# Performance work log

Hardware: AMD Instinct MI355X
Metric: run time of the kernel (lower is better)

The kernel has to match this reference:

```python
import jax, jax.numpy as jnp
import numpy as np

N_STATE = 4      # d_state from CrossMambaFusionBlock(d_state=4)
DT_RANK = 48     # ceil(768/16), standard Mamba dt_rank='auto'
D_CONV = 4       # depthwise causal conv kernel size


def _ln(x, g, b):
    m = jnp.mean(x, axis=-1, keepdims=True)
    v = jnp.mean((x - m) ** 2, axis=-1, keepdims=True)
    return (x - m) * jax.lax.rsqrt(v + 1e-5) * g + b


def _dwconv1d(u, w, b):
    # u: (B,L,D); w: (D,1,K) depthwise causal conv along token dim L
    K = w.shape[-1]
    up = jnp.pad(jnp.transpose(u, (0, 2, 1)), ((0, 0), (0, 0), (K - 1, 0)))
    out = jax.lax.conv_general_dilated(up, w, (1,), 'VALID',
                                       feature_group_count=w.shape[0],
                                       dimension_numbers=('NCH', 'OIH', 'NCH'))
    return jnp.transpose(out, (0, 2, 1)) + b


def _pre(x, g, b, Win, Wconv, bconv, Wxp, Wdt, bdt):
    # LayerNorm -> in_proj -> depthwise conv + SiLU -> dt/B/C projections
    B_, H, W, C = x.shape
    xn = _ln(x, g, b).reshape(B_, H * W, C)
    u, z = jnp.split(xn @ Win, 2, axis=-1)              # (B,L,D) each
    u = jax.nn.silu(_dwconv1d(u, Wconv, bconv))
    dbl = u @ Wxp                                        # (B,L,R+2N)
    dtr, Bm, Cm = jnp.split(dbl, [DT_RANK, DT_RANK + N_STATE], axis=-1)
    dt = jax.nn.softplus(dtr @ Wdt + bdt)                # (B,L,D)
    return u, z, dt, Bm, Cm


def _selective_scan(u, dt, Alog, Bm, Cm, Dskip):
    # u, dt: (B,L,D); Alog: (D,N); Bm, Cm: (B,L,N)
    A = -jnp.exp(Alog)
    dA = jnp.exp(dt[..., None] * A)                      # (B,L,D,N) decay
    dBu = (dt * u)[..., None] * Bm[:, :, None, :]        # (B,L,D,N) input

    def comb(c1, c2):
        a1, h1 = c1
        a2, h2 = c2
        return a1 * a2, a2 * h1 + h2

    _, h = jax.lax.associative_scan(comb, (dA, dBu), axis=1)
    return jnp.einsum('bldn,bln->bld', h, Cm) + u * Dskip


def _forward(x1, x2,
             ln_g1, ln_b1, Win1, Wconv1, bconv1, Wxp1, Wdt1, bdt1, Alog1, Dskip1, Wout1,
             ln_g2, ln_b2, Win2, Wconv2, bconv2, Wxp2, Wdt2, bdt2, Alog2, Dskip2, Wout2):
    x1 = jnp.transpose(x1, (0, 2, 3, 1))  # BCHW -> BHWC (as in forward_features)
    x2 = jnp.transpose(x2, (0, 2, 3, 1))
    B_, H, W, C = x1.shape
    u1, z1, dt1, B1, C1 = _pre(x1, ln_g1, ln_b1, Win1, Wconv1, bconv1, Wxp1, Wdt1, bdt1)
    u2, z2, dt2, B2, C2 = _pre(x2, ln_g2, ln_b2, Win2, Wconv2, bconv2, Wxp2, Wdt2, bdt2)
    # Cross-modal fusion: each stream's SSM state is read out with the OTHER
    # stream's C projection (cross selective scan).
    y1 = _selective_scan(u1, dt1, Alog1, B1, C2, Dskip1)
    y2 = _selective_scan(u2, dt2, Alog2, B2, C1, Dskip2)
    o1 = ((y1 * jax.nn.silu(z1)) @ Wout1).reshape(B_, H, W, C)
    o2 = ((y2 * jax.nn.silu(z2)) @ Wout2).reshape(B_, H, W, C)
    return x1 + o1, x2 + o2


def setup_inputs():
    key = jax.random.key(0)
    ks = jax.random.split(key, 16)
    B_, C, H, W = 2, 768, 64, 64
    D = C  # d_inner (ssm_ratio = 1)

    def nrm(k, shape, s=0.02):
        return jax.random.normal(k, shape, jnp.float32) * s

    inp = {
        'x1': jax.random.normal(ks[0], (B_, C, H, W), jnp.float32),
        'x2': jax.random.normal(ks[1], (B_, C, H, W), jnp.float32),
    }
    for i, o in ((1, 2), (2, 8)):
        inp[f'ln_g{i}'] = jnp.ones((C,), jnp.float32)
        inp[f'ln_b{i}'] = jnp.zeros((C,), jnp.float32)
        inp[f'Win{i}'] = nrm(ks[o], (C, 2 * D))
        inp[f'Wconv{i}'] = nrm(ks[o + 1], (D, 1, D_CONV), 0.1)
        inp[f'bconv{i}'] = jnp.zeros((D,), jnp.float32)
        inp[f'Wxp{i}'] = nrm(ks[o + 2], (D, DT_RANK + 2 * N_STATE))
        inp[f'Wdt{i}'] = nrm(ks[o + 3], (DT_RANK, D), 0.05)
        inp[f'bdt{i}'] = jnp.full((D,), -4.6, jnp.float32)  # softplus -> dt ~ 0.01
        inp[f'Alog{i}'] = jnp.log(jnp.broadcast_to(
            jnp.arange(1, N_STATE + 1, dtype=jnp.float32), (D, N_STATE)))
        inp[f'Dskip{i}'] = jnp.ones((D,), jnp.float32)
        inp[f'Wout{i}'] = nrm(ks[o + 4], (D, C))
    return inp


def reference(x1, x2,
              ln_g1, ln_b1, Win1, Wconv1, bconv1, Wxp1, Wdt1, bdt1, Alog1, Dskip1, Wout1,
              ln_g2, ln_b2, Win2, Wconv2, bconv2, Wxp2, Wdt2, bdt2, Alog2, Dskip2, Wout2):
    return _forward(x1, x2,
                    ln_g1, ln_b1, Win1, Wconv1, bconv1, Wxp1, Wdt1, bdt1, Alog1, Dskip1, Wout1,
                    ln_g2, ln_b2, Win2, Wconv2, bconv2, Wxp2, Wdt2, bdt2, Alog2, Dskip2, Wout2)
```

## Files before the change

### kernel.cpp

```cpp
#include <hip/hip_runtime.h>
#include <cmath>

#define LDIM 4096
#define CDIM 768
#define BDIM 2
#define NST 4
#define RNK 48
#define CH 64
#define LC 64
#define NDT 896

typedef short bf16x8 __attribute__((ext_vector_type(8)));
typedef float f32x4 __attribute__((ext_vector_type(4)));

__device__ __forceinline__ float sigmoidf_(float x) { return 1.f / (1.f + __expf(-x)); }

__device__ __forceinline__ unsigned short f2bf(float f) {
    unsigned int u = __float_as_uint(f);
    u += 0x7fffu + ((u >> 16) & 1u);
    return (unsigned short)(u >> 16);
}
__device__ __forceinline__ float bf2f(unsigned short us) {
    unsigned int u = ((unsigned int)us) << 16;
    return __uint_as_float(u);
}

__device__ __forceinline__ void llds16(const unsigned short* g, unsigned short* l) {
    __builtin_amdgcn_global_load_lds(
        (const __attribute__((address_space(1))) unsigned int*)g,
        (__attribute__((address_space(3))) unsigned int*)l, 16, 0, 0);
}

__global__ __launch_bounds__(256) void stats_kernel(const float* __restrict__ x0,
                                                    const float* __restrict__ x1,
                                                    float* __restrict__ stats)
{
    int blk = blockIdx.x;
    int s = blk >> 7;
    int b = (blk >> 6) & 1;
    int l0 = (blk & 63) * 64;
    int wave = threadIdx.x >> 6, lane = threadIdx.x & 63;
    const float* x = s ? x1 : x0;
    const float* xp = x + ((size_t)b * CDIM) * LDIM + l0 + lane;
    float sm = 0.f, sq = 0.f;
    int cbeg = wave * 192;
#pragma unroll
    for (int i0 = 0; i0 < 192; i0 += 16) {
        float v[16];
#pragma unroll
        for (int j = 0; j < 16; j++) v[j] = xp[(size_t)(cbeg + i0 + j) * LDIM];
#pragma unroll
        for (int j = 0; j < 16; j++) { sm += v[j]; sq += v[j] * v[j]; }
    }
    __shared__ float red[2][4][64];
    red[0][wave][lane] = sm;
    red[1][wave][lane] = sq;
    __syncthreads();
    if (wave == 0) {
        float s_ = red[0][0][lane] + red[0][1][lane] + red[0][2][lane] + red[0][3][lane];
        float q_ = red[1][0][lane] + red[1][1][lane] + red[1][2][lane] + red[1][3][lane];
        float m = s_ * (1.f / CDIM);
        float var = q_ * (1.f / CDIM) - m * m;
        int idx = s * 8192 + b * LDIM + l0 + lane;
        stats[2 * idx] = m;
        stats[2 * idx + 1] = rsqrtf(var + 1e-5f);
    }
}

__global__ __launch_bounds__(256) void transpose_ln_kernel(
    const float* __restrict__ x0, const float* __restrict__ x1,
    const float* __restrict__ g0, const float* __restrict__ bb0,
    const float* __restrict__ g1, const float* __restrict__ bb1,
    const float* __restrict__ stats,
    unsigned short* __restrict__ xnb0, unsigned short* __restrict__ xnb1,
    float* __restrict__ out)
{
    __shared__ float tile[64][65];
    int t = threadIdx.x;
    int c0 = blockIdx.x * 64, l0 = blockIdx.y * 64;
    int z = blockIdx.z;
    int s = z >> 1, b = z & 1;
    const float* x = s ? x1 : x0;
    const float* g = s ? g1 : g0;
    const float* bb = s ? bb1 : bb0;
    unsigned short* xnb = s ? xnb1 : xnb0;
    int tl = t & 63, tg = t >> 6;
#pragma unroll
    for (int i = 0; i < 16; i++) {
        int cl = tg * 16 + i;
        tile[cl][tl] = x[((size_t)(b * CDIM + c0 + cl)) * LDIM + l0 + tl];
    }
    __syncthreads();
    const size_t SZ = (size_t)BDIM * LDIM * CDIM;
#pragma unroll
    for (int i = 0; i < 16; i++) {
        int ll = tg * 16 + i;
        int l = l0 + ll, c = c0 + tl;
        float v = tile[tl][ll];
        int sidx = s * 8192 + b * LDIM + l;
        float m = stats[sidx * 2], rs = stats[sidx * 2 + 1];
        size_t o = ((size_t)(b * LDIM + l)) * CDIM + c;
        out[(size_t)s * SZ + o] = v;
        xnb[o] = f2bf((v - m) * rs * g[c] + bb[c]);
    }
}

__global__ __launch_bounds__(256) void wt_transpose_all(
    const float* __restrict__ Win0, const float* __restrict__ Win1,
    const float* __restrict__ Wout0, const float* __restrict__ Wout1,
    unsigned short* __restrict__ WinT0, unsigned short* __restrict__ WinT1,
    unsigned short* __restrict__ WoutT0, unsigned short* __restrict__ WoutT1)
{
    int z = blockIdx.z;
    const float* W = (z == 0) ? Win0 : (z == 1) ? Win1 : (z == 2) ? Wout0 : Wout1;
    unsigned short* Wt = (z == 0) ? WinT0 : (z == 1) ? WinT1 : (z == 2) ? WoutT0 : WoutT1;
    const int K = CDIM;
    const int N = (z < 2) ? 2 * CDIM : CDIM;
    if (blockIdx.x * 64 >= N) return;
    __shared__ float tile[64][65];
    int t = threadIdx.x;
    int n0 = blockIdx.x * 64, k0 = blockIdx.y * 64;
    int tn = t & 63, tg = t >> 6;
#pragma unroll
    for (int i = 0; i < 16; i++) {
        int kl = tg * 16 + i;
        tile[kl][tn] = W[(size_t)(k0 + kl) * N + n0 + tn];
    }
    __syncthreads();
#pragma unroll
    for (int i = 0; i < 16; i++) {
        int nl = tg * 16 + i;
        int k = k0 + tn, n = n0 + nl;
        Wt[(size_t)n * K + k] = f2bf(tile[tn][nl]);
    }
}

__global__ __launch_bounds__(256) void wcomb_kernel(
    const float* __restrict__ Wxp0, const float* __restrict__ Wdt0,
    const float* __restrict__ Wxp1, const float* __restrict__ Wdt1,
    unsigned short* __restrict__ W0, unsigned short* __restrict__ W1)
{
    int s = blockIdx.z;
    const float* Wxp = s ? Wxp1 : Wxp0;
    const float* Wdt = s ? Wdt1 : Wdt0;
    unsigned short* WcombT = s ? W1 : W0;
    int t = threadIdx.x;
    int k = blockIdx.x * 64 + (t & 63);
    int n0 = blockIdx.y * 64;
    float wx[RNK];
#pragma unroll
    for (int r = 0; r < RNK; r++) wx[r] = Wxp[k * 56 + r];
    for (int i = (t >> 6); i < 64; i += 4) {
        int n = n0 + i;
        float val;
        if (n < CDIM) {
            float acc = 0.f;
#pragma unroll
            for (int r = 0; r < RNK; r++) acc += wx[r] * Wdt[(size_t)r * CDIM + n];
            val = acc;
        } else if (n < CDIM + 8) {
            val = Wxp[k * 56 + RNK + (n - CDIM)];
        } else {
            val = 0.f;
        }
        WcombT[(size_t)n * CDIM + k] = f2bf(val);
    }
}

__global__ __launch_bounds__(512, 4) void gemm_mfma(
    const unsigned short* __restrict__ A0, const unsigned short* __restrict__ A1,
    const unsigned short* __restrict__ Bt0, const unsigned short* __restrict__ Bt1,
    void* __restrict__ C0, void* __restrict__ C1, int ldc, int K, int epi,
    const float* __restrict__ bias0, const float* __restrict__ bias1,
    float* __restrict__ D0, float* __restrict__ D1)
{
    const unsigned short* A = blockIdx.z ? A1 : A0;
    const unsigned short* Bt = blockIdx.z ? Bt1 : Bt0;
    void* C = blockIdx.z ? C1 : C0;
    const float* bias = blockIdx.z ? bias1 : bias0;
    float* D = blockIdx.z ? D1 : D0;

    __shared__ unsigned short As[3][128 * 32];
    __shared__ unsigned short Bs[3][128 * 32];
    const int tid = threadIdx.x;
    const int wave = tid >> 6, lane = tid & 63;
    const int row0 = blockIdx.x * 128, col0 = blockIdx.y * 128;
    const int wm = (wave >> 2) * 64, wn = (wave & 3) * 32;
    f32x4 acc[4][2] = {};
    const int lr = lane >> 2;
    const int gi = ((lane & 3) ^ ((lane >> 3) & 3)) * 8;
    const int fr = lane & 15, fc = lane >> 4;

    const unsigned short* ga0 = A + (size_t)(row0 + wave * 16 + lr) * K + gi;
    const unsigned short* gb0 = Bt + (size_t)(col0 + wave * 16 + lr) * K + gi;
    const int rb = wave * 16;

#define ISSUE(st, kb)                         \
    do {                                      \
        llds16(ga0 + (kb), &As[st][rb * 32]); \
        llds16(gb0 + (kb), &Bs[st][rb * 32]); \
    } while (0)

    const int NIT = K / 32;
    ISSUE(0, 0);
    ISSUE(1, 32);
    for (int i = 0; i < NIT; i++) {
        if (i < NIT - 1) __builtin_amdgcn_s_waitcnt(0xF72);
        else __builtin_amdgcn_s_waitcnt(0xF70);
        __builtin_amdgcn_s_barrier();
        if (i + 2 < NIT) ISSUE((i + 2) % 3, (i + 2) * 32);
        const unsigned short* as = As[i % 3];
        const unsigned short* bs = Bs[i % 3];
        bf16x8 af[4], bfr[2];
#pragma unroll
        for (int ii = 0; ii < 4; ii++) {
            int r = wm + ii * 16 + fr;
            af[ii] = *(const bf16x8*)&as[r * 32 + (fc ^ ((r >> 1) & 3)) * 8];
        }
#pragma unroll
        for (int j = 0; j < 2; j++) {
            int r = wn + j * 16 + fr;
            bfr[j] = *(const bf16x8*)&bs[r * 32 + (fc ^ ((r >> 1) & 3)) * 8];
        }
#pragma unroll
        for (int ii = 0; ii < 4; ii++)
#pragma unroll
            for (int j = 0; j < 2; j++)
                acc[ii][j] = __builtin_amdgcn_mfma_f32_16x16x32_bf16(af[ii], bfr[j], acc[ii][j], 0, 0, 0);
    }
#undef ISSUE

    const int cr = (lane >> 4) * 4, cc = lane & 15;
#pragma unroll
    for (int ii = 0; ii < 4; ii++)
#pragma unroll
        for (int j = 0; j < 2; j++) {
            int col = col0 + wn + j * 16 + cc;
#pragma unroll
            for (int r = 0; r < 4; r++) {
                int row = row0 + wm + ii * 16 + cr + r;
                float v = acc[ii][j][r];
                if (epi == 1) {
                    float* Cf = (float*)C;
                    size_t o = (size_t)row * ldc + col;
                    Cf[o] = v + Cf[o];
                } else if (epi == 2) {
                    if (col < CDIM) {
                        v += bias[col];
                        v = (v > 20.f) ? v : __logf(1.f + __expf(v));
                        ((unsigned short*)C)[(size_t)row * ldc + col] = f2bf(v);
                    } else if (col < CDIM + 8) {
                        D[(size_t)row * 8 + (col - CDIM)] = v;
                    }
                } else {
                    ((unsigned short*)C)[(size_t)row * ldc + col] = f2bf(v);
                }
            }
        }
}

__global__ __launch_bounds__(256) void conv_silu_kernel(
    const unsigned short* __restrict__ uzb0, const unsigned short* __restrict__ uzb1,
    const float* __restrict__ w0, const float* __restrict__ bc0,
    const float* __restrict__ w1, const float* __restrict__ bc1,
    unsigned short* __restrict__ ub0, unsigned short* __restrict__ ub1)
{
    int s = blockIdx.y;
    const unsigned short* uzb = s ? uzb1 : uzb0;
    const float* w = s ? w1 : w0;
    const float* bc = s ? bc1 : bc0;
    unsigned short* ub = s ? ub1 : ub0;
    int idx = blockIdx.x * 256 + threadIdx.x;
    int d8 = (idx % 96) * 8;
    int bl = idx / 96;
    int l = bl & (LDIM - 1);

    float wr[8][4];
#pragma unroll
    for (int q = 0; q < 8; q++) {
        f32x4 wv = *(const f32x4*)&w[(d8 + q) * 4];
#pragma unroll
        for (int k = 0; k < 4; k++) wr[q][k] = wv[k];
    }
    float acc[8];
    f32x4 b0 = *(const f32x4*)&bc[d8];
    f32x4 b1 = *(const f32x4*)&bc[d8 + 4];
#pragma unroll
    for (int q = 0; q < 4; q++) { acc[q] = b0[q]; acc[4 + q] = b1[q]; }

#pragma unroll
    for (int k = 0; k < 4; k++) {
        int ls = l - 3 + k;
        if (ls >= 0) {
            bf16x8 uv = *(const bf16x8*)&uzb[(size_t)(bl - 3 + k) * (2 * CDIM) + d8];
#pragma unroll
            for (int q = 0; q < 8; q++)
                acc[q] += bf2f((unsigned short)uv[q]) * wr[q][k];
        }
    }
    bf16x8 ov;
#pragma unroll
    for (int q = 0; q < 8; q++) {
        float v = acc[q];
        ov[q] = (short)f2bf(v * sigmoidf_(v));
    }
    *(bf16x8*)&ub[(size_t)bl * CDIM + d8] = ov;
}

__global__ __launch_bounds__(256) void scan_phaseA(
    const unsigned short* __restrict__ u0, const unsigned short* __restrict__ dt0,
    const float* __restrict__ dbl0, const float* __restrict__ Alog0,
    const unsigned short* __restrict__ u1, const unsigned short* __restrict__ dt1,
    const float* __restrict__ dbl1, const float* __restrict__ Alog1,
    float* __restrict__ agg)
{
    int idx = blockIdx.x * 256 + threadIdx.x;
    int d = idx % CDIM;
    int t1 = idx / CDIM;
    int c = t1 % CH;
    int t2 = t1 / CH;
    int b = t2 & 1;
    int s = t2 >> 1;
    const unsigned short* u = s ? u1 : u0;
    const unsigned short* dt = s ? dt1 : dt0;
    const float* dbl = s ? dbl1 : dbl0;
    const float* Alog = s ? Alog1 : Alog0;
    float A[4];
#pragma unroll
    for (int n = 0; n < 4; n++) A[n] = -__expf(Alog[d * 4 + n]);
    float h[4] = {0, 0, 0, 0}, aa[4] = {1, 1, 1, 1};
    int rowb = b * LDIM + c * LC;
    for (int t = 0; t < LC; t++) {
        int row = rowb + t;
        float dtv = bf2f(dt[(size_t)row * CDIM + d]);
        float uv = bf2f(u[(size_t)row * CDIM + d]);
        float du = dtv * uv;
        const float* bm = dbl + (size_t)row * 8;
#pragma unroll
        for (int n = 0; n < 4; n++) {
            float dA = __expf(dtv * A[n]);
            h[n] = dA * h[n] + du * bm[n];
            aa[n] *= dA;
        }
    }
    float* o = agg + (size_t)idx * 8;
#pragma unroll
    for (int n = 0; n < 4; n++) { o[n] = aa[n]; o[4 + n] = h[n]; }
}

__global__ __launch_bounds__(256) void scan_phaseB(const float* __restrict__ agg,
                                                   float* __restrict__ hinit)
{
    int idx = blockIdx.x * 256 + threadIdx.x;
    int d = idx % CDIM;
    int sb = idx / CDIM;
    float st[4] = {0, 0, 0, 0};
    for (int c = 0; c < CH; c++) {
        size_t base = ((size_t)sb * CH + c) * CDIM + d;
        const float* a = agg + base * 8;
        float* hi = hinit + base * 4;
#pragma unroll
        for (int n = 0; n < 4; n++) hi[n] = st[n];
#pragma unroll
        for (int n = 0; n < 4; n++) st[n] = a[n] * st[n] + a[4 + n];
    }
}

__global__ __launch_bounds__(256) void scan_phaseC(
    const unsigned short* __restrict__ u0, const unsigned short* __restrict__ dt0,
    const unsigned short* __restrict__ uzb0, const float* __restrict__ dbl0,
    const float* __restrict__ Alog0, const float* __restrict__ Dsk0, unsigned short* __restrict__ g0,
    const unsigned short* __restrict__ u1, const unsigned short* __restrict__ dt1,
    const unsigned short* __restrict__ uzb1, const float* __restrict__ dbl1,
    const float* __restrict__ Alog1, const float* __restrict__ Dsk1, unsigned short* __restrict__ g1,
    const float* __restrict__ hinit)
{
    int idx = blockIdx.x * 256 + threadIdx.x;
    int d = idx % CDIM;
    int t1 = idx / CDIM;
    int c = t1 % CH;
    int t2 = t1 / CH;
    int b = t2 & 1;
    int s = t2 >> 1;
    const unsigned short* u = s ? u1 : u0;
    const unsigned short* dt = s ? dt1 : dt0;
    const unsigned short* uzb = s ? uzb1 : uzb0;
    const float* dbl = s ? dbl1 : dbl0;
    const float* dblO = s ? dbl0 : dbl1;
    const float* Alog = s ? Alog1 : Alog0;
    const float* Dsk = s ? Dsk1 : Dsk0;
    unsigned short* gated = s ? g1 : g0;
    float A[4];
#pragma unroll
    for (int n = 0; n < 4; n++) A[n] = -__expf(Alog[d * 4 + n]);
    float Dv = Dsk[d];
    float h[4];
    const float* hi = hinit + (size_t)idx * 4;
#pragma unroll
    for (int n = 0; n < 4; n++) h[n] = hi[n];
    int rowb = b * LDIM + c * LC;
    for (int t = 0; t < LC; t++) {
        int row = rowb + t;
        float dtv = bf2f(dt[(size_t)row * CDIM + d]);
        float uv = bf2f(u[(size_t)row * CDIM + d]);
        float du = dtv * uv;
        const float* bm = dbl + (size_t)row * 8;
        const float* cm = dblO + (size_t)row * 8 + 4;
        float y = 0.f;
#pragma unroll
        for (int n = 0; n < 4; n++) {
            float dA = __expf(dtv * A[n]);
            h[n] = dA * h[n] + du * bm[n];
            y += h[n] * cm[n];
        }
        y += uv * Dv;
        float zv = bf2f(uzb[(size_t)row * (2 * CDIM) + CDIM + d]);
        gated[(size_t)row * CDIM + d] = f2bf(y * (zv * sigmoidf_(zv)));
    }
}

extern "C" void kernel_launch(void* const* d_in, const int* in_sizes, int n_in,
                              void* d_out, int out_size, void* d_ws, size_t ws_size,
                              hipStream_t stream)
{
    const float* x[2] = {(const float*)d_in[0], (const float*)d_in[1]};
    const float *ln_g[2], *ln_b[2], *Win[2], *Wconv[2], *bconv[2], *Wxp[2],
        *Wdt[2], *bdt[2], *Alog[2], *Dskip[2], *Wout[2];
    for (int s = 0; s < 2; s++) {
        int base = 2 + s * 11;
        ln_g[s] = (const float*)d_in[base + 0];
        ln_b[s] = (const float*)d_in[base + 1];
        Win[s] = (const float*)d_in[base + 2];
        Wconv[s] = (const float*)d_in[base + 3];
        bconv[s] = (const float*)d_in[base + 4];
        Wxp[s] = (const float*)d_in[base + 5];
        Wdt[s] = (const float*)d_in[base + 6];
        bdt[s] = (const float*)d_in[base + 7];
        Alog[s] = (const float*)d_in[base + 8];
        Dskip[s] = (const float*)d_in[base + 9];
        Wout[s] = (const float*)d_in[base + 10];
    }

    const int M = BDIM * LDIM;
    char* base = (char*)d_ws;
    auto alloc = [&](size_t bytes) {
        char* p = base;
        base += (bytes + 255) & ~(size_t)255;
        return p;
    };
    unsigned short* uzb[2] = {(unsigned short*)alloc((size_t)M * 1536 * 2),
                              (unsigned short*)alloc((size_t)M * 1536 * 2)};
    unsigned short* dtb[2] = {(unsigned short*)alloc((size_t)M * CDIM * 2),
                              (unsigned short*)alloc((size_t)M * CDIM * 2)};
    unsigned short* ub[2] = {(unsigned short*)alloc((size_t)M * CDIM * 2),
                             (unsigned short*)alloc((size_t)M * CDIM * 2)};
    unsigned short* xnb[2] = {(unsigned short*)alloc((size_t)M * CDIM * 2),
                              (unsigned short*)alloc((size_t)M * CDIM * 2)};
    float* dbl[2] = {(float*)alloc((size_t)M * 8 * 4), (float*)alloc((size_t)M * 8 * 4)};
    unsigned short* WinT[2] = {(unsigned short*)alloc(1536 * 768 * 2),
                               (unsigned short*)alloc(1536 * 768 * 2)};
    unsigned short* WoutT[2] = {(unsigned short*)alloc(768 * 768 * 2),
                                (unsigned short*)alloc(768 * 768 * 2)};
    unsigned short* WcombT[2] = {(unsigned short*)alloc((size_t)NDT * 768 * 2),
                                 (unsigned short*)alloc((size_t)NDT * 768 * 2)};
    float* agg = (float*)alloc((size_t)2 * BDIM * CH * CDIM * 8 * 4);
    float* hinit = (float*)alloc((size_t)2 * BDIM * CH * CDIM * 4 * 4);
    float* stats = (float*)alloc((size_t)2 * M * 2 * 4);

    dim3 blk(256);
    dim3 blk512(512);
    const size_t SZ = (size_t)BDIM * LDIM * CDIM;

    stats_kernel<<<dim3(256), blk, 0, stream>>>(x[0], x[1], stats);
    transpose_ln_kernel<<<dim3(CDIM / 64, LDIM / 64, 4), blk, 0, stream>>>(
        x[0], x[1], ln_g[0], ln_b[0], ln_g[1], ln_b[1], stats, xnb[0], xnb[1], (float*)d_out);

    wt_transpose_all<<<dim3(1536 / 64, 768 / 64, 4), blk, 0, stream>>>(
        Win[0], Win[1], Wout[0], Wout[1], WinT[0], WinT[1], WoutT[0], WoutT[1]);
    wcomb_kernel<<<dim3(768 / 64, NDT / 64, 2), blk, 0, stream>>>(
        Wxp[0], Wdt[0], Wxp[1], Wdt[1], WcombT[0], WcombT[1]);

    gemm_mfma<<<dim3(M / 128, 1536 / 128, 2), blk512, 0, stream>>>(
        xnb[0], xnb[1], WinT[0], WinT[1], uzb[0], uzb[1], 2 * CDIM, CDIM, 3,
        nullptr, nullptr, nullptr, nullptr);

    conv_silu_kernel<<<dim3((M * CDIM / 8) / 256, 2), blk, 0, stream>>>(
        uzb[0], uzb[1], Wconv[0], bconv[0], Wconv[1], bconv[1], ub[0], ub[1]);

    gemm_mfma<<<dim3(M / 128, NDT / 128, 2), blk512, 0, stream>>>(
        ub[0], ub[1], WcombT[0], WcombT[1], dtb[0], dtb[1], CDIM, CDIM, 2,
        bdt[0], bdt[1], dbl[0], dbl[1]);

    scan_phaseA<<<dim3((2 * BDIM * CH * CDIM) / 256), blk, 0, stream>>>(
        ub[0], dtb[0], dbl[0], Alog[0], ub[1], dtb[1], dbl[1], Alog[1], agg);
    scan_phaseB<<<dim3((2 * BDIM * CDIM) / 256), blk, 0, stream>>>(agg, hinit);
    scan_phaseC<<<dim3((2 * BDIM * CH * CDIM) / 256), blk, 0, stream>>>(
        ub[0], dtb[0], uzb[0], dbl[0], Alog[0], Dskip[0], xnb[0],
        ub[1], dtb[1], uzb[1], dbl[1], Alog[1], Dskip[1], xnb[1], hinit);

    float* out = (float*)d_out;
    gemm_mfma<<<dim3(M / 128, CDIM / 128, 2), blk512, 0, stream>>>(
        xnb[0], xnb[1], WoutT[0], WoutT[1], out, out + SZ, CDIM, CDIM, 1,
        nullptr, nullptr, nullptr, nullptr);
}
```

Baseline: 435.0 us.

## Merge prep kernels, vectorize transpose loads, and process two channels per scan thread

Folds the stats, weight-transpose and combined-weight kernels into one prep launch dispatched by block index, cutting two kernel launches. The LayerNorm transpose kernel now reads x with 16-byte vector loads instead of scalar loads. The scan phase A and C kernels each handle two adjacent channels per thread using 32-bit packed bf16 loads and stores, which halves the thread count and amortizes the per-row B/C loads. The scan changes lower parallelism, which may reduce latency hiding in the scans.

Measured after the change: 423.7 us. 1.03x faster.

```diff
diff --git a/kernel.cpp b/kernel.cpp
--- a/kernel.cpp
+++ b/kernel.cpp
@@ -24,6 +24,8 @@
     unsigned int u = ((unsigned int)us) << 16;
     return __uint_as_float(u);
 }
+__device__ __forceinline__ float bf2f_lo(unsigned int p) { return __uint_as_float(p << 16); }
+__device__ __forceinline__ float bf2f_hi(unsigned int p) { return __uint_as_float(p & 0xffff0000u); }
 
 __device__ __forceinline__ void llds16(const unsigned short* g, unsigned short* l) {
     __builtin_amdgcn_global_load_lds(
@@ -31,39 +33,103 @@
         (__attribute__((address_space(3))) unsigned int*)l, 16, 0, 0);
 }
 
-__global__ __launch_bounds__(256) void stats_kernel(const float* __restrict__ x0,
-                                                    const float* __restrict__ x1,
-                                                    float* __restrict__ stats)
-{
-    int blk = blockIdx.x;
-    int s = blk >> 7;
-    int b = (blk >> 6) & 1;
-    int l0 = (blk & 63) * 64;
-    int wave = threadIdx.x >> 6, lane = threadIdx.x & 63;
-    const float* x = s ? x1 : x0;
-    const float* xp = x + ((size_t)b * CDIM) * LDIM + l0 + lane;
-    float sm = 0.f, sq = 0.f;
-    int cbeg = wave * 192;
-#pragma unroll
-    for (int i0 = 0; i0 < 192; i0 += 16) {
-        float v[16];
-#pragma unroll
-        for (int j = 0; j < 16; j++) v[j] = xp[(size_t)(cbeg + i0 + j) * LDIM];
-#pragma unroll
-        for (int j = 0; j < 16; j++) { sm += v[j]; sq += v[j] * v[j]; }
-    }
-    __shared__ float red[2][4][64];
-    red[0][wave][lane] = sm;
-    red[1][wave][lane] = sq;
-    __syncthreads();
-    if (wave == 0) {
-        float s_ = red[0][0][lane] + red[0][1][lane] + red[0][2][lane] + red[0][3][lane];
-        float q_ = red[1][0][lane] + red[1][1][lane] + red[1][2][lane] + red[1][3][lane];
-        float m = s_ * (1.f / CDIM);
-        float var = q_ * (1.f / CDIM) - m * m;
-        int idx = s * 8192 + b * LDIM + l0 + lane;
-        stats[2 * idx] = m;
-        stats[2 * idx + 1] = rsqrtf(var + 1e-5f);
+__global__ __launch_bounds__(256) void prep_kernel(
+    const float* __restrict__ x0, const float* __restrict__ x1, float* __restrict__ stats,
+    const float* __restrict__ Win0, const float* __restrict__ Win1,
+    const float* __restrict__ Wout0, const float* __restrict__ Wout1,
+    unsigned short* __restrict__ WinT0, unsigned short* __restrict__ WinT1,
+    unsigned short* __restrict__ WoutT0, unsigned short* __restrict__ WoutT1,
+    const float* __restrict__ Wxp0, const float* __restrict__ Wdt0,
+    const float* __restrict__ Wxp1, const float* __restrict__ Wdt1,
+    unsigned short* __restrict__ Wc0, unsigned short* __restrict__ Wc1)
+{
+    __shared__ float smem[64 * 65];
+    int bid = blockIdx.x;
+    int t = threadIdx.x;
+
+    if (bid < 256) {
+        int s = bid >> 7;
+        int b = (bid >> 6) & 1;
+        int l0 = (bid & 63) * 64;
+        int wave = t >> 6, lane = t & 63;
+        const float* x = s ? x1 : x0;
+        const float* xp = x + ((size_t)b * CDIM) * LDIM + l0 + lane;
+        float sm = 0.f, sq = 0.f;
+        int cbeg = wave * 192;
+#pragma unroll
+        for (int i0 = 0; i0 < 192; i0 += 16) {
+            float v[16];
+#pragma unroll
+            for (int j = 0; j < 16; j++) v[j] = xp[(size_t)(cbeg + i0 + j) * LDIM];
+#pragma unroll
+            for (int j = 0; j < 16; j++) { sm += v[j]; sq += v[j] * v[j]; }
+        }
+        float* red = smem;
+        red[(0 * 4 + wave) * 64 + lane] = sm;
+        red[(1 * 4 + wave) * 64 + lane] = sq;
+        __syncthreads();
+        if (wave == 0) {
+            float s_ = red[lane] + red[64 + lane] + red[128 + lane] + red[192 + lane];
+            float q_ = red[256 + lane] + red[320 + lane] + red[384 + lane] + red[448 + lane];
+            float m = s_ * (1.f / CDIM);
+            float var = q_ * (1.f / CDIM) - m * m;
+            int idx = s * 8192 + b * LDIM + l0 + lane;
+            stats[2 * idx] = m;
+            stats[2 * idx + 1] = rsqrtf(var + 1e-5f);
+        }
+        return;
+    }
+    if (bid < 1408) {
+        int b2 = bid - 256;
+        int bx = b2 % 24, by = (b2 / 24) % 12, z = b2 / 288;
+        const float* W = (z == 0) ? Win0 : (z == 1) ? Win1 : (z == 2) ? Wout0 : Wout1;
+        unsigned short* Wt = (z == 0) ? WinT0 : (z == 1) ? WinT1 : (z == 2) ? WoutT0 : WoutT1;
+        const int K = CDIM;
+        const int N = (z < 2) ? 2 * CDIM : CDIM;
+        if (bx * 64 >= N) return;
+        float (*tile)[65] = (float(*)[65])smem;
+        int n0 = bx * 64, k0 = by * 64;
+        int tn = t & 63, tg = t >> 6;
+#pragma unroll
+        for (int i = 0; i < 16; i++) {
+            int kl = tg * 16 + i;
+            tile[kl][tn] = W[(size_t)(k0 + kl) * N + n0 + tn];
+        }
+        __syncthreads();
+#pragma unroll
+        for (int i = 0; i < 16; i++) {
+            int nl = tg * 16 + i;
+            int k = k0 + tn, n = n0 + nl;
+            Wt[(size_t)n * K + k] = f2bf(tile[tn][nl]);
+        }
+        return;
+    }
+    {
+        int b3 = bid - 1408;
+        int bx = b3 % 12, by = (b3 / 12) % 14, s = b3 / 168;
+        const float* Wxp = s ? Wxp1 : Wxp0;
+        const float* Wdt = s ? Wdt1 : Wdt0;
+        unsigned short* WcombT = s ? Wc1 : Wc0;
+        int k = bx * 64 + (t & 63);
+        int n0 = by * 64;
+        float wx[RNK];
+#pragma unroll
+        for (int r = 0; r < RNK; r++) wx[r] = Wxp[k * 56 + r];
+        for (int i = (t >> 6); i < 64; i += 4) {
+            int n = n0 + i;
+            float val;
+            if (n < CDIM) {
+                float acc = 0.f;
+#pragma unroll
+                for (int r = 0; r < RNK; r++) acc += wx[r] * Wdt[(size_t)r * CDIM + n];
+                val = acc;
+            } else if (n < CDIM + 8) {
+                val = Wxp[k * 56 + RNK + (n - CDIM)];
+            } else {
+                val = 0.f;
+            }
+            WcombT[(size_t)n * CDIM + k] = f2bf(val);
+        }
     }
 }
 
@@ -84,14 +150,17 @@
     const float* g = s ? g1 : g0;
     const float* bb = s ? bb1 : bb0;
     unsigned short* xnb = s ? xnb1 : xnb0;
-    int tl = t & 63, tg = t >> 6;
-#pragma unroll
-    for (int i = 0; i < 16; i++) {
-        int cl = tg * 16 + i;
-        tile[cl][tl] = x[((size_t)(b * CDIM + c0 + cl)) * LDIM + l0 + tl];
+    int lane16 = t & 15, cg = t >> 4;
+#pragma unroll
+    for (int i = 0; i < 4; i++) {
+        int cl = cg + 16 * i;
+        f32x4 v = *(const f32x4*)&x[((size_t)(b * CDIM + c0 + cl)) * LDIM + l0 + lane16 * 4];
+#pragma unroll
+        for (int j = 0; j < 4; j++) tile[cl][lane16 * 4 + j] = v[j];
     }
     __syncthreads();
     const size_t SZ = (size_t)BDIM * LDIM * CDIM;
+    int tl = t & 63, tg = t >> 6;
 #pragma unroll
     for (int i = 0; i < 16; i++) {
         int ll = tg * 16 + i;
@@ -102,68 +171,6 @@
         size_t o = ((size_t)(b * LDIM + l)) * CDIM + c;
         out[(size_t)s * SZ + o] = v;
         xnb[o] = f2bf((v - m) * rs * g[c] + bb[c]);
-    }
-}
-
-__global__ __launch_bounds__(256) void wt_transpose_all(
-    const float* __restrict__ Win0, const float* __restrict__ Win1,
-    const float* __restrict__ Wout0, const float* __restrict__ Wout1,
-    unsigned short* __restrict__ WinT0, unsigned short* __restrict__ WinT1,
-    unsigned short* __restrict__ WoutT0, unsigned short* __restrict__ WoutT1)
-{
-    int z = blockIdx.z;
-    const float* W = (z == 0) ? Win0 : (z == 1) ? Win1 : (z == 2) ? Wout0 : Wout1;
-    unsigned short* Wt = (z == 0) ? WinT0 : (z == 1) ? WinT1 : (z == 2) ? WoutT0 : WoutT1;
-    const int K = CDIM;
-    const int N = (z < 2) ? 2 * CDIM : CDIM;
-    if (blockIdx.x * 64 >= N) return;
-    __shared__ float tile[64][65];
-    int t = threadIdx.x;
-    int n0 = blockIdx.x * 64, k0 = blockIdx.y * 64;
-    int tn = t & 63, tg = t >> 6;
-#pragma unroll
-    for (int i = 0; i < 16; i++) {
-        int kl = tg * 16 + i;
-        tile[kl][tn] = W[(size_t)(k0 + kl) * N + n0 + tn];
-    }
-    __syncthreads();
-#pragma unroll
-    for (int i = 0; i < 16; i++) {
-        int nl = tg * 16 + i;
-        int k = k0 + tn, n = n0 + nl;
-        Wt[(size_t)n * K + k] = f2bf(tile[tn][nl]);
-    }
-}
-
-__global__ __launch_bounds__(256) void wcomb_kernel(
-    const float* __restrict__ Wxp0, const float* __restrict__ Wdt0,
-    const float* __restrict__ Wxp1, const float* __restrict__ Wdt1,
-    unsigned short* __restrict__ W0, unsigned short* __restrict__ W1)
-{
-    int s = blockIdx.z;
-    const float* Wxp = s ? Wxp1 : Wxp0;
-    const float* Wdt = s ? Wdt1 : Wdt0;
-    unsigned short* WcombT = s ? W1 : W0;
-    int t = threadIdx.x;
-    int k = blockIdx.x * 64 + (t & 63);
-    int n0 = blockIdx.y * 64;
-    float wx[RNK];
-#pragma unroll
-    for (int r = 0; r < RNK; r++) wx[r] = Wxp[k * 56 + r];
-    for (int i = (t >> 6); i < 64; i += 4) {
-        int n = n0 + i;
-        float val;
-        if (n < CDIM) {
-            float acc = 0.f;
-#pragma unroll
-            for (int r = 0; r < RNK; r++) acc += wx[r] * Wdt[(size_t)r * CDIM + n];
-            val = acc;
-        } else if (n < CDIM + 8) {
-            val = Wxp[k * 56 + RNK + (n - CDIM)];
-        } else {
-            val = 0.f;
-        }
-        WcombT[(size_t)n * CDIM + k] = f2bf(val);
     }
 }
 
@@ -315,8 +322,9 @@
     float* __restrict__ agg)
 {
     int idx = blockIdx.x * 256 + threadIdx.x;
-    int d = idx % CDIM;
-    int t1 = idx / CDIM;
+    int dp = idx % 384;
+    int d0 = dp * 2;
+    int t1 = idx / 384;
     int c = t1 % CH;
     int t2 = t1 / CH;
     int b = t2 & 1;
@@ -325,27 +333,42 @@
     const unsigned short* dt = s ? dt1 : dt0;
     const float* dbl = s ? dbl1 : dbl0;
     const float* Alog = s ? Alog1 : Alog0;
-    float A[4];
-#pragma unroll
-    for (int n = 0; n < 4; n++) A[n] = -__expf(Alog[d * 4 + n]);
-    float h[4] = {0, 0, 0, 0}, aa[4] = {1, 1, 1, 1};
+    float A[2][4];
+#pragma unroll
+    for (int j = 0; j < 2; j++)
+#pragma unroll
+        for (int n = 0; n < 4; n++) A[j][n] = -__expf(Alog[(d0 + j) * 4 + n]);
+    float h[2][4] = {}, aa[2][4];
+#pragma unroll
+    for (int j = 0; j < 2; j++)
+#pragma unroll
+        for (int n = 0; n < 4; n++) aa[j][n] = 1.f;
     int rowb = b * LDIM + c * LC;
     for (int t = 0; t < LC; t++) {
         int row = rowb + t;
-        float dtv = bf2f(dt[(size_t)row * CDIM + d]);
-        float uv = bf2f(u[(size_t)row * CDIM + d]);
-        float du = dtv * uv;
+        unsigned int up = *(const unsigned int*)&u[(size_t)row * CDIM + d0];
+        unsigned int dp2 = *(const unsigned int*)&dt[(size_t)row * CDIM + d0];
+        float uv[2] = {bf2f_lo(up), bf2f_hi(up)};
+        float dtv[2] = {bf2f_lo(dp2), bf2f_hi(dp2)};
         const float* bm = dbl + (size_t)row * 8;
 #pragma unroll
-        for (int n = 0; n < 4; n++) {
-            float dA = __expf(dtv * A[n]);
-            h[n] = dA * h[n] + du * bm[n];
-            aa[n] *= dA;
-        }
-    }
-    float* o = agg + (size_t)idx * 8;
-#pragma unroll
-    for (int n = 0; n < 4; n++) { o[n] = aa[n]; o[4 + n] = h[n]; }
+        for (int j = 0; j < 2; j++) {
+            float du = dtv[j] * uv[j];
+#pragma unroll
+            for (int n = 0; n < 4; n++) {
+                float dA = __expf(dtv[j] * A[j][n]);
+                h[j][n] = dA * h[j][n] + du * bm[n];
+                aa[j][n] *= dA;
+            }
+        }
+    }
+    size_t base = ((size_t)(s * 2 + b) * CH + c) * CDIM + d0;
+#pragma unroll
+    for (int j = 0; j < 2; j++) {
+        float* o = agg + (base + j) * 8;
+#pragma unroll
+        for (int n = 0; n < 4; n++) { o[n] = aa[j][n]; o[4 + n] = h[j][n]; }
+    }
 }
 
 __global__ __launch_bounds__(256) void scan_phaseB(const float* __restrict__ agg,
@@ -376,8 +399,9 @@
     const float* __restrict__ hinit)
 {
     int idx = blockIdx.x * 256 + threadIdx.x;
-    int d = idx % CDIM;
-    int t1 = idx / CDIM;
+    int dp = idx % 384;
+    int d0 = dp * 2;
+    int t1 = idx / 384;
     int c = t1 % CH;
     int t2 = t1 / CH;
     int b = t2 & 1;
@@ -390,32 +414,47 @@
     const float* Alog = s ? Alog1 : Alog0;
     const float* Dsk = s ? Dsk1 : Dsk0;
     unsigned short* gated = s ? g1 : g0;
-    float A[4];
-#pragma unroll
-    for (int n = 0; n < 4; n++) A[n] = -__expf(Alog[d * 4 + n]);
-    float Dv = Dsk[d];
-    float h[4];
-    const float* hi = hinit + (size_t)idx * 4;
-#pragma unroll
-    for (int n = 0; n < 4; n++) h[n] = hi[n];
+    float A[2][4];
+#pragma unroll
+    for (int j = 0; j < 2; j++)
+#pragma unroll
+        for (int n = 0; n < 4; n++) A[j][n] = -__expf(Alog[(d0 + j) * 4 + n]);
+    float Dv[2] = {Dsk[d0], Dsk[d0 + 1]};
+    float h[2][4];
+    size_t base = ((size_t)(s * 2 + b) * CH + c) * CDIM + d0;
+#pragma unroll
+    for (int j = 0; j < 2; j++) {
+        const float* hi = hinit + (base + j) * 4;
+#pragma unroll
+        for (int n = 0; n < 4; n++) h[j][n] = hi[n];
+    }
     int rowb = b * LDIM + c * LC;
     for (int t = 0; t < LC; t++) {
         int row = rowb + t;
-        float dtv = bf2f(dt[(size_t)row * CDIM + d]);
-        float uv = bf2f(u[(size_t)row * CDIM + d]);
-        float du = dtv * uv;
+        unsigned int up = *(const unsigned int*)&u[(size_t)row * CDIM + d0];
+        unsigned int dp2 = *(const unsigned int*)&dt[(size_t)row * CDIM + d0];
+        unsigned int zp = *(const unsigned int*)&uzb[(size_t)row * (2 * CDIM) + CDIM + d0];
+        float uv[2] = {bf2f_lo(up), bf2f_hi(up)};
+        float dtv[2] = {bf2f_lo(dp2), bf2f_hi(dp2)};
+        float zv[2] = {bf2f_lo(zp), bf2f_hi(zp)};
         const float* bm = dbl + (size_t)row * 8;
         const float* cm = dblO + (size_t)row * 8 + 4;
-        float y = 0.f;
-#pragma unroll
-        for (int n = 0; n < 4; n++) {
-            float dA = __expf(dtv * A[n]);
-            h[n] = dA * h[n] + du * bm[n];
-            y += h[n] * cm[n];
-        }
-        y += uv * Dv;
-        float zv = bf2f(uzb[(size_t)row * (2 * CDIM) + CDIM + d]);
-        gated[(size_t)row * CDIM + d] = f2bf(y * (zv * sigmoidf_(zv)));
+        unsigned int outp = 0;
+#pragma unroll
+        for (int j = 0; j < 2; j++) {
+            float du = dtv[j] * uv[j];
+            float y = 0.f;
+#pragma unroll
+            for (int n = 0; n < 4; n++) {
+                float dA = __expf(dtv[j] * A[j][n]);
+                h[j][n] = dA * h[j][n] + du * bm[n];
+                y += h[j][n] * cm[n];
+            }
+            y += uv[j] * Dv[j];
+            unsigned short gb = f2bf(y * (zv[j] * sigmoidf_(zv[j])));
+            outp |= ((unsigned int)gb) << (16 * j);
+        }
+        *(unsigned int*)&gated[(size_t)row * CDIM + d0] = outp;
     }
 }
 
@@ -471,14 +510,13 @@
     dim3 blk512(512);
     const size_t SZ = (size_t)BDIM * LDIM * CDIM;
 
-    stats_kernel<<<dim3(256), blk, 0, stream>>>(x[0], x[1], stats);
+    prep_kernel<<<dim3(1744), blk, 0, stream>>>(
+        x[0], x[1], stats,
+        Win[0], Win[1], Wout[0], Wout[1], WinT[0], WinT[1], WoutT[0], WoutT[1],
+        Wxp[0], Wdt[0], Wxp[1], Wdt[1], WcombT[0], WcombT[1]);
+
     transpose_ln_kernel<<<dim3(CDIM / 64, LDIM / 64, 4), blk, 0, stream>>>(
         x[0], x[1], ln_g[0], ln_b[0], ln_g[1], ln_b[1], stats, xnb[0], xnb[1], (float*)d_out);
-
-    wt_transpose_all<<<dim3(1536 / 64, 768 / 64, 4), blk, 0, stream>>>(
-        Win[0], Win[1], Wout[0], Wout[1], WinT[0], WinT[1], WoutT[0], WoutT[1]);
-    wcomb_kernel<<<dim3(768 / 64, NDT / 64, 2), blk, 0, stream>>>(
-        Wxp[0], Wdt[0], Wxp[1], Wdt[1], WcombT[0], WcombT[1]);
 
     gemm_mfma<<<dim3(M / 128, 1536 / 128, 2), blk512, 0, stream>>>(
         xnb[0], xnb[1], WinT[0], WinT[1], uzb[0], uzb[1], 2 * CDIM, CDIM, 3,
@@ -491,10 +529,10 @@
         ub[0], ub[1], WcombT[0], WcombT[1], dtb[0], dtb[1], CDIM, CDIM, 2,
         bdt[0], bdt[1], dbl[0], dbl[1]);
 
-    scan_phaseA<<<dim3((2 * BDIM * CH * CDIM) / 256), blk, 0, stream>>>(
+    scan_phaseA<<<dim3((2 * BDIM * CH * (CDIM / 2)) / 256), blk, 0, stream>>>(
         ub[0], dtb[0], dbl[0], Alog[0], ub[1], dtb[1], dbl[1], Alog[1], agg);
     scan_phaseB<<<dim3((2 * BDIM * CDIM) / 256), blk, 0, stream>>>(agg, hinit);
-    scan_phaseC<<<dim3((2 * BDIM * CH * CDIM) / 256), blk, 0, stream>>>(
+    scan_phaseC<<<dim3((2 * BDIM * CH * (CDIM / 2)) / 256), blk, 0, stream>>>(
         ub[0], dtb[0], uzb[0], dbl[0], Alog[0], Dskip[0], xnb[0],
         ub[1], dtb[1], uzb[1], dbl[1], Alog[1], Dskip[1], xnb[1], hinit);
 
```
